# Kernel tuning notes

Measured on AMD Instinct MI355X. Metric: run time of the kernel, lower is better.

The kernel has to match this reference:

```python
import jax, jax.numpy as jnp
import numpy as np

NUM_CLASSES = 2
LOG2_NC = float(np.log2(NUM_CLASSES))


def _conv(x, w, b=None):
    # NCHW conv, stride 1, SAME padding (kernel 3 pad 1 or kernel 1 pad 0)
    y = jax.lax.conv_general_dilated(x, w, (1, 1), 'SAME',
                                     dimension_numbers=('NCHW', 'OIHW', 'NCHW'))
    if b is not None:
        y = y + b[None, :, None, None]
    return y


def _uncertainty_map(ds):
    # entropy over class dim, thresholded to {0,1}
    logp = jax.nn.log_softmax(ds, axis=1)            # [B,C,H,W]
    prob = jnp.exp(logp)
    # torch uses log2(prob + 1e-6); replicate exactly
    ent = -jnp.sum(prob * jnp.log2(prob + 1e-6), axis=1) / LOG2_NC  # [B,H,W]
    return (ent >= 0.001).astype(jnp.float32)


def _unob(tar, amap):
    # vectorized UnoB with S=3: interior pixels with tar!=0 get pro=0 unless
    # 4*tar == sum of the 4-neighborhood (i.e. locally constant label)
    t = tar  # [B,H,W] int
    nb = t[:, 2:, 1:-1] + t[:, :-2, 1:-1] + t[:, 1:-1, 2:] + t[:, 1:-1, :-2]
    center = t[:, 1:-1, 1:-1]
    inner_pro = jnp.where((center != 0) & (4 * center != nb), 0.0, 1.0)
    pro = jnp.ones_like(amap)
    pro = pro.at[:, 1:-1, 1:-1].set(inner_pro)
    return amap * pro


def setup_inputs() -> dict:
    key = jax.random.key(0)
    ks = jax.random.split(key, 6)
    B, C, H, W = 8, 128, 128, 128
    return {
        'x': jax.random.normal(ks[0], (B, C, H, W), jnp.float32),
        'skip': jax.random.normal(ks[1], (B, C, H, W), jnp.float32),
        'tar': jax.random.randint(ks[2], (B, 1, H, W), 0, NUM_CLASSES, jnp.int64)
            if jax.config.jax_enable_x64 else
            jax.random.randint(ks[2], (B, 1, H, W), 0, NUM_CLASSES).astype(jnp.int32),
        'W1': jax.random.normal(ks[3], (128, 256, 3, 3), jnp.float32) * 0.05,
        'b1': jnp.zeros((128,), jnp.float32),
        'W2': jax.random.normal(ks[4], (128, 128, 3, 3), jnp.float32) * 0.05,
        'b2': jnp.zeros((128,), jnp.float32),
        'Wds': jax.random.normal(ks[5], (NUM_CLASSES, 128, 1, 1), jnp.float32) * 0.05,
    }


def reference(x, skip, tar, W1, b1, W2, b2, Wds):
    h = jnp.concatenate([x, skip], axis=1)            # [B,2*dim,H,W]
    h = jax.nn.leaky_relu(_conv(h, W1, b1), 0.01)     # [B,dim,H,W]
    h = jax.nn.leaky_relu(_conv(h, W2, b2), 0.01)
    ds = _conv(h, Wds)                                # [B,num_classes,H,W]
    amap = _uncertainty_map(ds)                       # [B,H,W]
    amap = _unob(tar[:, 0], amap)                     # UnoB refinement, S=3
    return h, ds, amap
```

## Files before the change

### kernel.cpp

```cpp
#include <hip/hip_runtime.h>

typedef float f32x16 __attribute__((ext_vector_type(16)));
typedef short bf16x8 __attribute__((ext_vector_type(8)));
typedef unsigned int u32;

static __device__ __forceinline__ unsigned short f2bf(float f) {
  union { float f; unsigned int u; } v;
  v.f = f;
  return (unsigned short)((v.u + 0x7FFFu + ((v.u >> 16) & 1u)) >> 16);
}

static __device__ __forceinline__ void gl_lds16(const unsigned short* g,
                                                unsigned short* l) {
  __builtin_amdgcn_global_load_lds(
      (const __attribute__((address_space(1))) u32*)g,
      (__attribute__((address_space(3))) u32*)l, 16, 0, 0);
}

#define VMCNT8 asm volatile("s_waitcnt vmcnt(8)" ::: "memory")
#define VMCNT0 asm volatile("s_waitcnt vmcnt(0)" ::: "memory")
#define LGKM0 asm volatile("s_waitcnt lgkmcnt(0)" ::: "memory")
#define BAR __builtin_amdgcn_s_barrier()
#define SCHEDB __builtin_amdgcn_sched_barrier(0)
#define PRIO1 __builtin_amdgcn_s_setprio(1)
#define PRIO0 __builtin_amdgcn_s_setprio(0)

__global__ __launch_bounds__(256) void convert_weights(
    const float* __restrict__ W1, const float* __restrict__ W2,
    unsigned short* __restrict__ W1b, unsigned short* __restrict__ W2b,
    unsigned short* __restrict__ zp) {
  if (blockIdx.x == 1728) {
    uint4* z = (uint4*)zp;
    z[threadIdx.x] = make_uint4(0, 0, 0, 0);
    z[256 + threadIdx.x] = make_uint4(0, 0, 0, 0);
    return;
  }
  int i = blockIdx.x * 256 + threadIdx.x;
  if (i < 294912) {
    int e = i & 7, co = (i >> 3) & 127, r = i >> 10;
    int tap = r % 9, pc = r / 9;
    int ci = (pc >> 1) * 16 + (pc & 1) * 8 + e;
    W1b[i] = f2bf(W1[(co * 256 + ci) * 9 + tap]);
  } else {
    int j = i - 294912;
    if (j < 147456) {
      int e = j & 7, co = (j >> 3) & 127, r = j >> 10;
      int tap = r % 9, pc = r / 9;
      int ci = (pc >> 1) * 16 + (pc & 1) * 8 + e;
      W2b[j] = f2bf(W2[(co * 128 + ci) * 9 + tap]);
    }
  }
}

__global__ __launch_bounds__(256) void transpose_to_bf16(
    const float* __restrict__ src, unsigned short* __restrict__ dst, int cigb) {
  int row = blockIdx.x;
  int b = row >> 7, y = row & 127;
  const float* s = src + (long)b * 128 * 16384 + (long)y * 128;
  for (int it = 0; it < 8; ++it) {
    int u = it * 256 + (int)threadIdx.x;
    int cig = u >> 7, px = u & 127;
    unsigned short pk[8];
#pragma unroll
    for (int e = 0; e < 8; ++e)
      pk[e] = f2bf(s[(long)(cig * 8 + e) * 16384 + px]);
    uint4 vv;
    vv.x = (unsigned)pk[0] | ((unsigned)pk[1] << 16);
    vv.y = (unsigned)pk[2] | ((unsigned)pk[3] << 16);
    vv.z = (unsigned)pk[4] | ((unsigned)pk[5] << 16);
    vv.w = (unsigned)pk[6] | ((unsigned)pk[7] << 16);
    *(uint4*)(&dst[(((long)row * 32 + cigb + cig) * 130 + px + 1) * 8]) = vv;
  }
  if (cigb == 0 && threadIdx.x < 64) {
    int g = threadIdx.x >> 1;
    long col = (threadIdx.x & 1) * 129L;
    *(uint4*)(&dst[(((long)row * 32 + g) * 130 + col) * 8]) = make_uint4(0, 0, 0, 0);
  }
}

template <int CIN, bool FUSE_DS>
__global__ __launch_bounds__(512, 2) void conv3x3(
    const unsigned short* __restrict__ src,
    const unsigned short* __restrict__ wt,
    const float* __restrict__ bias,
    const unsigned short* __restrict__ zp,
    unsigned short* __restrict__ dst_bf16,
    float* __restrict__ dst_f32,
    const float* __restrict__ wds,
    const int* __restrict__ tar,
    float* __restrict__ ds,
    float* __restrict__ amap) {
  constexpr int CPG = CIN / 8;
  constexpr int NC = CIN / 16;
  __shared__ unsigned short in_tile[2][1664 * 8];
  __shared__ unsigned short wt_tile[2][2304 * 8];
  __shared__ unsigned short scr[64 * 8];
  __shared__ float sb[128];
  __shared__ float w0s[128], w1s[128];
  __shared__ float sc[4 * 4 * 2 * 32];

  const int tid = threadIdx.x;
  const int b = blockIdx.x >> 5;
  const int y0 = (blockIdx.x & 31) * 4;
  const int lane = tid & 63, wave = tid >> 6;
  const int wco = wave & 1, wrow = wave >> 1;
  const int l31 = lane & 31, kh = lane >> 5;

  if (tid < 128) {
    sb[tid] = bias[tid];
    if constexpr (FUSE_DS) {
      w0s[tid] = wds[tid];
      w1s[tid] = wds[128 + tid];
    }
  }

  const unsigned short* gb[8];
  unsigned short* ld0[8];
  int gst[8];
  int lst[8];
#pragma unroll
  for (int i = 0; i < 8; ++i) {
    const int o = wave * 8 + i;
    if (o < 36) {
      gb[i] = wt + o * 512 + lane * 8;
      gst[i] = 18432;
      ld0[i] = &wt_tile[0][(size_t)o * 512];
      lst[i] = 18432;
    } else if (o < 62) {
      const int q = o - 36;
      const int p = q / 13, j = q - p * 13;
      const int s = j * 64 + lane;
      const int hy = s / 130, hx = s - hy * 130;
      const int gy = y0 - 1 + hy;
      const bool ok = (s < 780) && (gy >= 0) && (gy < 128);
      gb[i] = ok ? src + ((size_t)((b * 128 + gy) * CPG) + p) * 1040 + hx * 8
                 : zp + lane * 8;
      gst[i] = ok ? 2080 : 0;
      ld0[i] = &in_tile[0][(size_t)(p * 832 + j * 64) * 8];
      lst[i] = 1664 * 8;
    } else {
      gb[i] = zp + lane * 8;
      gst[i] = 0;
      ld0[i] = &scr[0];
      lst[i] = 0;
    }
  }

  f32x16 acc[2][4] = {};

#pragma unroll
  for (int i = 0; i < 8; ++i) gl_lds16(gb[i], ld0[i]);
  VMCNT0;
  LGKM0;
  BAR;
  SCHEDB;

  for (int cic = 0; cic < NC; ++cic) {
    const int cur = cic & 1;
    const bool more = (cic + 1 < NC);
    if (more) {
      const int nb = cur ^ 1;
#pragma unroll
      for (int i = 0; i < 8; ++i)
        gl_lds16(gb[i] + (size_t)(cic + 1) * gst[i],
                 ld0[i] + (size_t)nb * lst[i]);
      SCHEDB;
      VMCNT8;
    } else {
      VMCNT0;
    }
    SCHEDB;
    BAR;
    SCHEDB;

    const unsigned short* it = &in_tile[cur][0];
    const unsigned short* wl = &wt_tile[cur][0];
    const size_t ib = (size_t)kh * (832 * 8);
    const size_t wb = (size_t)kh * 9216;

    bf16x8 xa0, xa1, xb0, xb1, xb2, xb3;
    bf16x8 ya0, ya1, yb0, yb1, yb2, yb3;

#define LD_TAP(T, A0, A1, B0, B1, B2, B3)                                      \
  {                                                                            \
    constexpr int ky_ = (T) / 3, kx_ = (T) % 3;                                \
    const int hy_ = ky_ + wrow;                                                \
    A0 = *(const bf16x8*)(&wl[wb + (size_t)((T)*128 + wco * 64 + l31) * 8]);   \
    A1 = *(const bf16x8*)(&wl[wb + (size_t)((T)*128 + wco * 64 + 32 + l31) * 8]); \
    B0 = *(const bf16x8*)(&it[ib + (size_t)(hy_ * 130 + l31 + kx_) * 8]);      \
    B1 = *(const bf16x8*)(&it[ib + (size_t)(hy_ * 130 + 32 + l31 + kx_) * 8]); \
    B2 = *(const bf16x8*)(&it[ib + (size_t)(hy_ * 130 + 64 + l31 + kx_) * 8]); \
    B3 = *(const bf16x8*)(&it[ib + (size_t)(hy_ * 130 + 96 + l31 + kx_) * 8]); \
  }

#define MFMA_TAP(A0, A1, B0, B1, B2, B3)                                       \
  {                                                                            \
    PRIO1;                                                                     \
    acc[0][0] = __builtin_amdgcn_mfma_f32_32x32x16_bf16(A0, B0, acc[0][0], 0, 0, 0); \
    acc[0][1] = __builtin_amdgcn_mfma_f32_32x32x16_bf16(A0, B1, acc[0][1], 0, 0, 0); \
    acc[0][2] = __builtin_amdgcn_mfma_f32_32x32x16_bf16(A0, B2, acc[0][2], 0, 0, 0); \
    acc[0][3] = __builtin_amdgcn_mfma_f32_32x32x16_bf16(A0, B3, acc[0][3], 0, 0, 0); \
    acc[1][0] = __builtin_amdgcn_mfma_f32_32x32x16_bf16(A1, B0, acc[1][0], 0, 0, 0); \
    acc[1][1] = __builtin_amdgcn_mfma_f32_32x32x16_bf16(A1, B1, acc[1][1], 0, 0, 0); \
    acc[1][2] = __builtin_amdgcn_mfma_f32_32x32x16_bf16(A1, B2, acc[1][2], 0, 0, 0); \
    acc[1][3] = __builtin_amdgcn_mfma_f32_32x32x16_bf16(A1, B3, acc[1][3], 0, 0, 0); \
    PRIO0;                                                                     \
  }

    LD_TAP(0, xa0, xa1, xb0, xb1, xb2, xb3);
    LD_TAP(1, ya0, ya1, yb0, yb1, yb2, yb3);
    SCHEDB;
    MFMA_TAP(xa0, xa1, xb0, xb1, xb2, xb3);
    LD_TAP(2, xa0, xa1, xb0, xb1, xb2, xb3);
    SCHEDB;
    MFMA_TAP(ya0, ya1, yb0, yb1, yb2, yb3);
    LD_TAP(3, ya0, ya1, yb0, yb1, yb2, yb3);
    SCHEDB;
    MFMA_TAP(xa0, xa1, xb0, xb1, xb2, xb3);
    LD_TAP(4, xa0, xa1, xb0, xb1, xb2, xb3);
    SCHEDB;
    MFMA_TAP(ya0, ya1, yb0, yb1, yb2, yb3);
    LD_TAP(5, ya0, ya1, yb0, yb1, yb2, yb3);
    SCHEDB;
    MFMA_TAP(xa0, xa1, xb0, xb1, xb2, xb3);
    LD_TAP(6, xa0, xa1, xb0, xb1, xb2, xb3);
    SCHEDB;
    MFMA_TAP(ya0, ya1, yb0, yb1, yb2, yb3);
    LD_TAP(7, ya0, ya1, yb0, yb1, yb2, yb3);
    SCHEDB;
    MFMA_TAP(xa0, xa1, xb0, xb1, xb2, xb3);
    LD_TAP(8, xa0, xa1, xb0, xb1, xb2, xb3);
    SCHEDB;
    MFMA_TAP(ya0, ya1, yb0, yb1, yb2, yb3);
    SCHEDB;
    MFMA_TAP(xa0, xa1, xb0, xb1, xb2, xb3);
#undef LD_TAP
#undef MFMA_TAP

    SCHEDB;
    LGKM0;
    BAR;
    SCHEDB;
  }

  const int gyo = y0 + wrow;
  float pd[4][2] = {};
#pragma unroll
  for (int fc = 0; fc < 2; ++fc) {
#pragma unroll
    for (int fp = 0; fp < 4; ++fp) {
      const int px = fp * 32 + l31;
      if constexpr (!FUSE_DS) {
#pragma unroll
        for (int rg = 0; rg < 4; ++rg) {
          const int co0 = wco * 64 + fc * 32 + rg * 8 + kh * 4;
          unsigned short pk[4];
#pragma unroll
          for (int q = 0; q < 4; ++q) {
            float v = acc[fc][fp][rg * 4 + q] + sb[co0 + q];
            v = v > 0.f ? v : 0.01f * v;
            pk[q] = f2bf(v);
          }
          uint2 o;
          o.x = (unsigned)pk[0] | ((unsigned)pk[1] << 16);
          o.y = (unsigned)pk[2] | ((unsigned)pk[3] << 16);
          *(uint2*)(&dst_bf16[(((long)(b * 128 + gyo) * 16 + (co0 >> 3)) * 130 + px + 1) * 8 +
                              kh * 4]) = o;
        }
      } else {
#pragma unroll
        for (int rg = 0; rg < 4; ++rg) {
          const int co0 = wco * 64 + fc * 32 + rg * 8 + kh * 4;
          float4 wv0 = *(const float4*)(&w0s[co0]);
          float4 wv1 = *(const float4*)(&w1s[co0]);
#pragma unroll
          for (int q = 0; q < 4; ++q) {
            float v = acc[fc][fp][rg * 4 + q] + sb[co0 + q];
            v = v > 0.f ? v : 0.01f * v;
            dst_f32[((long)(b * 128 + co0 + q) << 14) + (gyo << 7) + px] = v;
            float wq0 = (q == 0) ? wv0.x : (q == 1) ? wv0.y : (q == 2) ? wv0.z : wv0.w;
            float wq1 = (q == 0) ? wv1.x : (q == 1) ? wv1.y : (q == 2) ? wv1.z : wv1.w;
            pd[fp][0] += wq0 * v;
            pd[fp][1] += wq1 * v;
          }
        }
      }
    }
  }

  if constexpr (!FUSE_DS) {
    if (tid < 128) {
      int row = tid >> 5, g = (tid >> 1) & 15;
      long col = (tid & 1) * 129L;
      *(uint4*)(&dst_bf16[(((long)(b * 128 + y0 + row) * 16 + g) * 130 + col) * 8]) =
          make_uint4(0, 0, 0, 0);
    }
  } else {
#pragma unroll
    for (int fp = 0; fp < 4; ++fp)
#pragma unroll
      for (int c = 0; c < 2; ++c)
        pd[fp][c] += __shfl_xor(pd[fp][c], 32, 64);
    if (wco == 1 && kh == 0) {
#pragma unroll
      for (int fp = 0; fp < 4; ++fp)
#pragma unroll
        for (int c = 0; c < 2; ++c)
          sc[((wrow * 4 + fp) * 2 + c) * 32 + l31] = pd[fp][c];
    }
    __syncthreads();
    if (wco == 0 && kh == 0) {
      const int* tb = tar + (long)b * 16384;
#pragma unroll
      for (int fp = 0; fp < 4; ++fp) {
        const int px = fp * 32 + l31;
        float a0 = pd[fp][0] + sc[((wrow * 4 + fp) * 2 + 0) * 32 + l31];
        float a1 = pd[fp][1] + sc[((wrow * 4 + fp) * 2 + 1) * 32 + l31];
        ds[((long)b * 2) * 16384 + (gyo << 7) + px] = a0;
        ds[((long)b * 2 + 1) * 16384 + (gyo << 7) + px] = a1;
        float m = fmaxf(a0, a1);
        float e0 = expf(a0 - m), e1 = expf(a1 - m);
        float s = e0 + e1;
        float p0f = e0 / s, p1f = e1 / s;
        float ent = -(p0f * log2f(p0f + 1e-6f) + p1f * log2f(p1f + 1e-6f));
        float un = ent >= 0.001f ? 1.f : 0.f;
        float pro = 1.f;
        if (gyo > 0 && gyo < 127 && px > 0 && px < 127) {
          int c = tb[(gyo << 7) + px];
          if (c != 0) {
            int nb2 = tb[((gyo - 1) << 7) + px] + tb[((gyo + 1) << 7) + px] +
                      tb[(gyo << 7) + px - 1] + tb[(gyo << 7) + px + 1];
            if (4 * c != nb2) pro = 0.f;
          }
        }
        amap[((long)(b * 128 + gyo) << 7) + px] = un * pro;
      }
    }
  }
}

extern "C" void kernel_launch(void* const* d_in, const int* in_sizes, int n_in,
                              void* d_out, int out_size, void* d_ws, size_t ws_size,
                              hipStream_t stream) {
  const float* x    = (const float*)d_in[0];
  const float* skip = (const float*)d_in[1];
  const int*   tar  = (const int*)d_in[2];
  const float* W1   = (const float*)d_in[3];
  const float* b1   = (const float*)d_in[4];
  const float* W2   = (const float*)d_in[5];
  const float* b2   = (const float*)d_in[6];
  const float* Wds  = (const float*)d_in[7];

  float* out_h  = (float*)d_out;
  float* out_ds = out_h + 16777216;
  float* out_am = out_ds + 262144;

  unsigned short* W1b = (unsigned short*)d_ws;
  unsigned short* W2b = W1b + 294912;
  unsigned short* zp  = W2b + 147456;
  unsigned short* h1  = (unsigned short*)((char*)d_ws + (1u << 20));

  unsigned short* h0 = (unsigned short*)d_out;

  convert_weights<<<1729, 256, 0, stream>>>(W1, W2, W1b, W2b, zp);
  transpose_to_bf16<<<1024, 256, 0, stream>>>(x, h0, 0);
  transpose_to_bf16<<<1024, 256, 0, stream>>>(skip, h0, 16);
  conv3x3<256, false><<<256, 512, 0, stream>>>(h0, W1b, b1, zp, h1, nullptr,
                                               nullptr, nullptr, nullptr, nullptr);
  conv3x3<128, true><<<256, 512, 0, stream>>>(h1, W2b, b2, zp, nullptr, out_h,
                                              Wds, tar, out_ds, out_am);
}
```

Baseline: 149.3 us.

## Use four waves per block each covering all 128 output channels

The conv kernel drops from 8 waves (2 channel halves x 4 rows) to 4 waves, each computing a full 128x128 output tile per row with a 4x4 MFMA accumulator grid. B-operand (input) LDS reads are now shared across twice as many MFMAs, and the cross-wave LDS reduction plus __syncthreads in the fused ds epilogue go away. Each wave now issues 16 global-to-LDS loads per step, and the s_setprio hints are removed. The costs are doubled accumulator registers (256 VGPRs of accumulators), fewer waves per CU to hide latency, and more load work per thread.

```diff
diff --git a/kernel.cpp b/kernel.cpp
--- a/kernel.cpp
+++ b/kernel.cpp
@@ -17,13 +17,11 @@
       (__attribute__((address_space(3))) u32*)l, 16, 0, 0);
 }
 
-#define VMCNT8 asm volatile("s_waitcnt vmcnt(8)" ::: "memory")
+#define VMCNT16 asm volatile("s_waitcnt vmcnt(16)" ::: "memory")
 #define VMCNT0 asm volatile("s_waitcnt vmcnt(0)" ::: "memory")
 #define LGKM0 asm volatile("s_waitcnt lgkmcnt(0)" ::: "memory")
 #define BAR __builtin_amdgcn_s_barrier()
 #define SCHEDB __builtin_amdgcn_sched_barrier(0)
-#define PRIO1 __builtin_amdgcn_s_setprio(1)
-#define PRIO0 __builtin_amdgcn_s_setprio(0)
 
 __global__ __launch_bounds__(256) void convert_weights(
     const float* __restrict__ W1, const float* __restrict__ W2,
@@ -79,7 +77,7 @@
 }
 
 template <int CIN, bool FUSE_DS>
-__global__ __launch_bounds__(512, 2) void conv3x3(
+__global__ __launch_bounds__(256, 1) void conv3x3(
     const unsigned short* __restrict__ src,
     const unsigned short* __restrict__ wt,
     const float* __restrict__ bias,
@@ -97,13 +95,12 @@
   __shared__ unsigned short scr[64 * 8];
   __shared__ float sb[128];
   __shared__ float w0s[128], w1s[128];
-  __shared__ float sc[4 * 4 * 2 * 32];
 
   const int tid = threadIdx.x;
   const int b = blockIdx.x >> 5;
   const int y0 = (blockIdx.x & 31) * 4;
   const int lane = tid & 63, wave = tid >> 6;
-  const int wco = wave & 1, wrow = wave >> 1;
+  const int wrow = wave;
   const int l31 = lane & 31, kh = lane >> 5;
 
   if (tid < 128) {
@@ -114,13 +111,13 @@
     }
   }
 
-  const unsigned short* gb[8];
-  unsigned short* ld0[8];
-  int gst[8];
-  int lst[8];
-#pragma unroll
-  for (int i = 0; i < 8; ++i) {
-    const int o = wave * 8 + i;
+  const unsigned short* gb[16];
+  unsigned short* ld0[16];
+  int gst[16];
+  int lst[16];
+#pragma unroll
+  for (int i = 0; i < 16; ++i) {
+    const int o = wave * 16 + i;
     if (o < 36) {
       gb[i] = wt + o * 512 + lane * 8;
       gst[i] = 18432;
@@ -146,10 +143,10 @@
     }
   }
 
-  f32x16 acc[2][4] = {};
-
-#pragma unroll
-  for (int i = 0; i < 8; ++i) gl_lds16(gb[i], ld0[i]);
+  f32x16 acc[4][4] = {};
+
+#pragma unroll
+  for (int i = 0; i < 16; ++i) gl_lds16(gb[i], ld0[i]);
   VMCNT0;
   LGKM0;
   BAR;
@@ -161,11 +158,11 @@
     if (more) {
       const int nb = cur ^ 1;
 #pragma unroll
-      for (int i = 0; i < 8; ++i)
+      for (int i = 0; i < 16; ++i)
         gl_lds16(gb[i] + (size_t)(cic + 1) * gst[i],
                  ld0[i] + (size_t)nb * lst[i]);
       SCHEDB;
-      VMCNT8;
+      VMCNT16;
     } else {
       VMCNT0;
     }
@@ -178,24 +175,25 @@
     const size_t ib = (size_t)kh * (832 * 8);
     const size_t wb = (size_t)kh * 9216;
 
-    bf16x8 xa0, xa1, xb0, xb1, xb2, xb3;
-    bf16x8 ya0, ya1, yb0, yb1, yb2, yb3;
-
-#define LD_TAP(T, A0, A1, B0, B1, B2, B3)                                      \
+    bf16x8 xa0, xa1, xa2, xa3, xb0, xb1, xb2, xb3;
+    bf16x8 ya0, ya1, ya2, ya3, yb0, yb1, yb2, yb3;
+
+#define LD_TAP(T, A0, A1, A2, A3, B0, B1, B2, B3)                              \
   {                                                                            \
     constexpr int ky_ = (T) / 3, kx_ = (T) % 3;                                \
     const int hy_ = ky_ + wrow;                                                \
-    A0 = *(const bf16x8*)(&wl[wb + (size_t)((T)*128 + wco * 64 + l31) * 8]);   \
-    A1 = *(const bf16x8*)(&wl[wb + (size_t)((T)*128 + wco * 64 + 32 + l31) * 8]); \
+    A0 = *(const bf16x8*)(&wl[wb + (size_t)((T)*128 + l31) * 8]);              \
+    A1 = *(const bf16x8*)(&wl[wb + (size_t)((T)*128 + 32 + l31) * 8]);         \
+    A2 = *(const bf16x8*)(&wl[wb + (size_t)((T)*128 + 64 + l31) * 8]);         \
+    A3 = *(const bf16x8*)(&wl[wb + (size_t)((T)*128 + 96 + l31) * 8]);         \
     B0 = *(const bf16x8*)(&it[ib + (size_t)(hy_ * 130 + l31 + kx_) * 8]);      \
     B1 = *(const bf16x8*)(&it[ib + (size_t)(hy_ * 130 + 32 + l31 + kx_) * 8]); \
     B2 = *(const bf16x8*)(&it[ib + (size_t)(hy_ * 130 + 64 + l31 + kx_) * 8]); \
     B3 = *(const bf16x8*)(&it[ib + (size_t)(hy_ * 130 + 96 + l31 + kx_) * 8]); \
   }
 
-#define MFMA_TAP(A0, A1, B0, B1, B2, B3)                                       \
+#define MFMA_TAP(A0, A1, A2, A3, B0, B1, B2, B3)                               \
   {                                                                            \
-    PRIO1;                                                                     \
     acc[0][0] = __builtin_amdgcn_mfma_f32_32x32x16_bf16(A0, B0, acc[0][0], 0, 0, 0); \
     acc[0][1] = __builtin_amdgcn_mfma_f32_32x32x16_bf16(A0, B1, acc[0][1], 0, 0, 0); \
     acc[0][2] = __builtin_amdgcn_mfma_f32_32x32x16_bf16(A0, B2, acc[0][2], 0, 0, 0); \
@@ -204,36 +202,43 @@
     acc[1][1] = __builtin_amdgcn_mfma_f32_32x32x16_bf16(A1, B1, acc[1][1], 0, 0, 0); \
     acc[1][2] = __builtin_amdgcn_mfma_f32_32x32x16_bf16(A1, B2, acc[1][2], 0, 0, 0); \
     acc[1][3] = __builtin_amdgcn_mfma_f32_32x32x16_bf16(A1, B3, acc[1][3], 0, 0, 0); \
-    PRIO0;                                                                     \
-  }
-
-    LD_TAP(0, xa0, xa1, xb0, xb1, xb2, xb3);
-    LD_TAP(1, ya0, ya1, yb0, yb1, yb2, yb3);
-    SCHEDB;
-    MFMA_TAP(xa0, xa1, xb0, xb1, xb2, xb3);
-    LD_TAP(2, xa0, xa1, xb0, xb1, xb2, xb3);
-    SCHEDB;
-    MFMA_TAP(ya0, ya1, yb0, yb1, yb2, yb3);
-    LD_TAP(3, ya0, ya1, yb0, yb1, yb2, yb3);
-    SCHEDB;
-    MFMA_TAP(xa0, xa1, xb0, xb1, xb2, xb3);
-    LD_TAP(4, xa0, xa1, xb0, xb1, xb2, xb3);
-    SCHEDB;
-    MFMA_TAP(ya0, ya1, yb0, yb1, yb2, yb3);
-    LD_TAP(5, ya0, ya1, yb0, yb1, yb2, yb3);
-    SCHEDB;
-    MFMA_TAP(xa0, xa1, xb0, xb1, xb2, xb3);
-    LD_TAP(6, xa0, xa1, xb0, xb1, xb2, xb3);
-    SCHEDB;
-    MFMA_TAP(ya0, ya1, yb0, yb1, yb2, yb3);
-    LD_TAP(7, ya0, ya1, yb0, yb1, yb2, yb3);
-    SCHEDB;
-    MFMA_TAP(xa0, xa1, xb0, xb1, xb2, xb3);
-    LD_TAP(8, xa0, xa1, xb0, xb1, xb2, xb3);
-    SCHEDB;
-    MFMA_TAP(ya0, ya1, yb0, yb1, yb2, yb3);
-    SCHEDB;
-    MFMA_TAP(xa0, xa1, xb0, xb1, xb2, xb3);
+    acc[2][0] = __builtin_amdgcn_mfma_f32_32x32x16_bf16(A2, B0, acc[2][0], 0, 0, 0); \
+    acc[2][1] = __builtin_amdgcn_mfma_f32_32x32x16_bf16(A2, B1, acc[2][1], 0, 0, 0); \
+    acc[2][2] = __builtin_amdgcn_mfma_f32_32x32x16_bf16(A2, B2, acc[2][2], 0, 0, 0); \
+    acc[2][3] = __builtin_amdgcn_mfma_f32_32x32x16_bf16(A2, B3, acc[2][3], 0, 0, 0); \
+    acc[3][0] = __builtin_amdgcn_mfma_f32_32x32x16_bf16(A3, B0, acc[3][0], 0, 0, 0); \
+    acc[3][1] = __builtin_amdgcn_mfma_f32_32x32x16_bf16(A3, B1, acc[3][1], 0, 0, 0); \
+    acc[3][2] = __builtin_amdgcn_mfma_f32_32x32x16_bf16(A3, B2, acc[3][2], 0, 0, 0); \
+    acc[3][3] = __builtin_amdgcn_mfma_f32_32x32x16_bf16(A3, B3, acc[3][3], 0, 0, 0); \
+  }
+
+    LD_TAP(0, xa0, xa1, xa2, xa3, xb0, xb1, xb2, xb3);
+    LD_TAP(1, ya0, ya1, ya2, ya3, yb0, yb1, yb2, yb3);
+    SCHEDB;
+    MFMA_TAP(xa0, xa1, xa2, xa3, xb0, xb1, xb2, xb3);
+    LD_TAP(2, xa0, xa1, xa2, xa3, xb0, xb1, xb2, xb3);
+    SCHEDB;
+    MFMA_TAP(ya0, ya1, ya2, ya3, yb0, yb1, yb2, yb3);
+    LD_TAP(3, ya0, ya1, ya2, ya3, yb0, yb1, yb2, yb3);
+    SCHEDB;
+    MFMA_TAP(xa0, xa1, xa2, xa3, xb0, xb1, xb2, xb3);
+    LD_TAP(4, xa0, xa1, xa2, xa3, xb0, xb1, xb2, xb3);
+    SCHEDB;
+    MFMA_TAP(ya0, ya1, ya2, ya3, yb0, yb1, yb2, yb3);
+    LD_TAP(5, ya0, ya1, ya2, ya3, yb0, yb1, yb2, yb3);
+    SCHEDB;
+    MFMA_TAP(xa0, xa1, xa2, xa3, xb0, xb1, xb2, xb3);
+    LD_TAP(6, xa0, xa1, xa2, xa3, xb0, xb1, xb2, xb3);
+    SCHEDB;
+    MFMA_TAP(ya0, ya1, ya2, ya3, yb0, yb1, yb2, yb3);
+    LD_TAP(7, ya0, ya1, ya2, ya3, yb0, yb1, yb2, yb3);
+    SCHEDB;
+    MFMA_TAP(xa0, xa1, xa2, xa3, xb0, xb1, xb2, xb3);
+    LD_TAP(8, xa0, xa1, xa2, xa3, xb0, xb1, xb2, xb3);
+    SCHEDB;
+    MFMA_TAP(ya0, ya1, ya2, ya3, yb0, yb1, yb2, yb3);
+    SCHEDB;
+    MFMA_TAP(xa0, xa1, xa2, xa3, xb0, xb1, xb2, xb3);
 #undef LD_TAP
 #undef MFMA_TAP
 
@@ -246,14 +251,14 @@
   const int gyo = y0 + wrow;
   float pd[4][2] = {};
 #pragma unroll
-  for (int fc = 0; fc < 2; ++fc) {
+  for (int fc = 0; fc < 4; ++fc) {
 #pragma unroll
     for (int fp = 0; fp < 4; ++fp) {
       const int px = fp * 32 + l31;
       if constexpr (!FUSE_DS) {
 #pragma unroll
         for (int rg = 0; rg < 4; ++rg) {
-          const int co0 = wco * 64 + fc * 32 + rg * 8 + kh * 4;
+          const int co0 = fc * 32 + rg * 8 + kh * 4;
           unsigned short pk[4];
 #pragma unroll
           for (int q = 0; q < 4; ++q) {
@@ -270,7 +275,7 @@
       } else {
 #pragma unroll
         for (int rg = 0; rg < 4; ++rg) {
-          const int co0 = wco * 64 + fc * 32 + rg * 8 + kh * 4;
+          const int co0 = fc * 32 + rg * 8 + kh * 4;
           float4 wv0 = *(const float4*)(&w0s[co0]);
           float4 wv1 = *(const float4*)(&w1s[co0]);
 #pragma unroll
@@ -301,21 +306,13 @@
 #pragma unroll
       for (int c = 0; c < 2; ++c)
         pd[fp][c] += __shfl_xor(pd[fp][c], 32, 64);
-    if (wco == 1 && kh == 0) {
-#pragma unroll
-      for (int fp = 0; fp < 4; ++fp)
-#pragma unroll
-        for (int c = 0; c < 2; ++c)
-          sc[((wrow * 4 + fp) * 2 + c) * 32 + l31] = pd[fp][c];
-    }
-    __syncthreads();
-    if (wco == 0 && kh == 0) {
+    if (kh == 0) {
       const int* tb = tar + (long)b * 16384;
 #pragma unroll
       for (int fp = 0; fp < 4; ++fp) {
         const int px = fp * 32 + l31;
-        float a0 = pd[fp][0] + sc[((wrow * 4 + fp) * 2 + 0) * 32 + l31];
-        float a1 = pd[fp][1] + sc[((wrow * 4 + fp) * 2 + 1) * 32 + l31];
+        float a0 = pd[fp][0];
+        float a1 = pd[fp][1];
         ds[((long)b * 2) * 16384 + (gyo << 7) + px] = a0;
         ds[((long)b * 2 + 1) * 16384 + (gyo << 7) + px] = a1;
         float m = fmaxf(a0, a1);
@@ -365,8 +362,8 @@
   convert_weights<<<1729, 256, 0, stream>>>(W1, W2, W1b, W2b, zp);
   transpose_to_bf16<<<1024, 256, 0, stream>>>(x, h0, 0);
   transpose_to_bf16<<<1024, 256, 0, stream>>>(skip, h0, 16);
-  conv3x3<256, false><<<256, 512, 0, stream>>>(h0, W1b, b1, zp, h1, nullptr,
+  conv3x3<256, false><<<256, 256, 0, stream>>>(h0, W1b, b1, zp, h1, nullptr,
                                                nullptr, nullptr, nullptr, nullptr);
-  conv3x3<128, true><<<256, 512, 0, stream>>>(h1, W2b, b2, zp, nullptr, out_h,
+  conv3x3<128, true><<<256, 256, 0, stream>>>(h1, W2b, b2, zp, nullptr, out_h,
                                               Wds, tar, out_ds, out_am);
 }
```

Result: slower. 156.9 us (+5.1%).
